# Kernel tuning notes

Hardware: AMD Instinct MI355X
Metric: run time of the kernel (lower is better)

The kernel has to match this reference:

```python
import jax, jax.numpy as jnp
import numpy as np

BM = 192          # query-group block size (kernel assert: mbm == 192)
TOPK = 896        # round(0.3 * n / 64) * 64 selected keys per query group
RAND_ONE_IN = 100


def setup_inputs() -> dict:
    key = jax.random.key(0)
    kq, kk, kv = jax.random.split(key, 3)
    b, h, n, d = 1, 24, 3072, 128
    q = jax.random.normal(kq, (b, h, n, d), dtype=jnp.float32)
    k = jax.random.normal(kk, (b, h, n, d), dtype=jnp.float32)
    v = jax.random.normal(kv, (b, h, n, d), dtype=jnp.float32)
    return {"q": q, "k": k, "v": v}


def reference(q, k, v):
    b, h, n, d = q.shape
    qg = n // BM
    scale = 1.0 / np.sqrt(d).astype(np.float32)
    # dense attention (dense_colsum_attn): output + per-query-group column sums
    s = jnp.einsum('bhqd,bhkd->bhqk', q, k) * scale          # [b,h,n,n]
    p = jax.nn.softmax(s, axis=-1)
    o = jnp.einsum('bhqk,bhkd->bhqd', p, v)                  # dense output
    cs = p.reshape(b, h, qg, BM, n).sum(axis=3)              # block colsums [b,h,qg,n]
    rmask = jax.random.randint(jax.random.key(1), cs.shape, 0, RAND_ONE_IN) == 0
    idx = jax.lax.top_k(cs, TOPK)[1]                         # [b,h,qg,TOPK]
    flat = rmask.reshape(-1, n)
    rows = jnp.arange(flat.shape[0])[:, None]
    mask = flat.at[rows, idx.reshape(-1, TOPK)].set(True).reshape(b, h, qg, n)
    # csp_attn: block-sparse attention, each BM-query group attends only to masked keys
    sg = s.reshape(b, h, qg, BM, n)
    neg = jnp.finfo(s.dtype).min
    sp_p = jax.nn.softmax(jnp.where(mask[:, :, :, None, :], sg, neg), axis=-1)
    sp = jnp.einsum('bhgmk,bhkd->bhgmd', sp_p, v).reshape(b, h, n, d)
    # full step returns o; out_cache (stored for sparse steps) is o - sp
    return jnp.stack([o, o - sp])  # [2,b,h,n,d]
```

## Files before the change

### kernel.cpp

```cpp
#include <hip/hip_runtime.h>
#include <math.h>

#define H  24
#define NN 3072
#define D  128
#define G  16
#define BM 192
#define TOPK_K 896
#define PST 34
#define OUT2_OFF ((size_t)H * NN * D)
#define KV_HALF_BYTES ((size_t)H * NN * D * 2)
#define CSD_BYTES ((size_t)H * G * NN * 8)

#define LOG2E_SCALE 0.12751743822f

typedef _Float16 half8 __attribute__((ext_vector_type(8)));
typedef _Float16 half4v __attribute__((ext_vector_type(4)));
typedef __fp16 fp16x2 __attribute__((ext_vector_type(2)));
typedef float floatx4 __attribute__((ext_vector_type(4)));

#define GLOAD_LDS(g, l) __builtin_amdgcn_global_load_lds( \
    (const __attribute__((address_space(1))) void*)(g),   \
    (__attribute__((address_space(3))) void*)(l), 16, 0, 0)
#define WAITVM(N) asm volatile("s_waitcnt vmcnt(" #N ")" ::: "memory")

__device__ __forceinline__ floatx4 fzero4() {
  floatx4 z = {0.f, 0.f, 0.f, 0.f};
  return z;
}
__device__ __forceinline__ half8 pack_h8_rte(float4 a, float4 b) {
  half8 r;
  r[0] = (_Float16)a.x; r[1] = (_Float16)a.y; r[2] = (_Float16)a.z; r[3] = (_Float16)a.w;
  r[4] = (_Float16)b.x; r[5] = (_Float16)b.y; r[6] = (_Float16)b.z; r[7] = (_Float16)b.w;
  return r;
}
__device__ __forceinline__ half8 pack_h8_rtz(float4 a, float4 b) {
  fp16x2 h0 = __builtin_amdgcn_cvt_pkrtz(a.x, a.y);
  fp16x2 h1 = __builtin_amdgcn_cvt_pkrtz(a.z, a.w);
  fp16x2 h2 = __builtin_amdgcn_cvt_pkrtz(b.x, b.y);
  fp16x2 h3 = __builtin_amdgcn_cvt_pkrtz(b.z, b.w);
  half8 r;
  r[0] = (_Float16)h0[0]; r[1] = (_Float16)h0[1];
  r[2] = (_Float16)h1[0]; r[3] = (_Float16)h1[1];
  r[4] = (_Float16)h2[0]; r[5] = (_Float16)h2[1];
  r[6] = (_Float16)h3[0]; r[7] = (_Float16)h3[1];
  return r;
}
__device__ __forceinline__ half8 pack_h8_residual(float4 a, float4 b, half8 hi) {
  float4 ra = make_float4(a.x - (float)hi[0], a.y - (float)hi[1],
                          a.z - (float)hi[2], a.w - (float)hi[3]);
  float4 rb = make_float4(b.x - (float)hi[4], b.y - (float)hi[5],
                          b.z - (float)hi[6], b.w - (float)hi[7]);
  return pack_h8_rte(ra, rb);
}

__device__ __forceinline__ void tf2x32(unsigned k0, unsigned k1, unsigned x0, unsigned x1,
                                       unsigned* o0, unsigned* o1) {
  unsigned ks2 = k0 ^ k1 ^ 0x1BD11BDAu;
  unsigned v0 = x0 + k0, v1 = x1 + k1;
#define TF_RND(r) { v0 += v1; v1 = (v1 << (r)) | (v1 >> (32 - (r))); v1 ^= v0; }
  TF_RND(13) TF_RND(15) TF_RND(26) TF_RND(6)   v0 += k1;  v1 += ks2 + 1u;
  TF_RND(17) TF_RND(29) TF_RND(16) TF_RND(24)  v0 += ks2; v1 += k0 + 2u;
  TF_RND(13) TF_RND(15) TF_RND(26) TF_RND(6)   v0 += k0;  v1 += k1 + 3u;
  TF_RND(17) TF_RND(29) TF_RND(16) TF_RND(24)  v0 += k1;  v1 += ks2 + 4u;
  TF_RND(13) TF_RND(15) TF_RND(26) TF_RND(6)   v0 += ks2; v1 += k0 + 5u;
#undef TF_RND
  *o0 = v0; *o1 = v1;
}

__global__ __launch_bounds__(256)
void rmask_kernel(float* __restrict__ mask) {
  const unsigned S = H * G * NN;
  unsigned i = blockIdx.x * 256u + threadIdx.x;
  if (i >= S) return;
  unsigned hb, lb, a, b;
  unsigned k1a, k1b, k2a, k2b;
  tf2x32(0u, 1u, 0u, 0u, &k1a, &k1b);
  tf2x32(0u, 1u, 0u, 1u, &k2a, &k2b);
  tf2x32(k1a, k1b, 0u, i, &a, &b); hb = a ^ b;
  tf2x32(k2a, k2b, 0u, i, &a, &b); lb = a ^ b;
  unsigned r = ((hb % 100u) * 96u + (lb % 100u)) % 100u;
  mask[i] = (r == 0u) ? 1.0f : 0.0f;
}

__global__ __launch_bounds__(256)
void cvt_k_kernel(const float* __restrict__ k, _Float16* __restrict__ khi,
                  _Float16* __restrict__ klo) {
  size_t i = (size_t)blockIdx.x * 256 + threadIdx.x;
  const float4* src = (const float4*)k + i * 2;
  float4 a = src[0], b = src[1];
  half8 hi = pack_h8_rte(a, b);
  *(half8*)(khi + i * 8) = hi;
  *(half8*)(klo + i * 8) = pack_h8_residual(a, b, hi);
}

__global__ __launch_bounds__(256)
void cvt_vT_kernel(const float* __restrict__ v, _Float16* __restrict__ vT) {
  __shared__ _Float16 t[64][68];
  const int h = blockIdx.z, k0 = blockIdx.x * 64, d0 = blockIdx.y * 64;
  const int tid = threadIdx.x;
  const int c4 = tid & 15, r = tid >> 4;
#pragma unroll
  for (int i = 0; i < 4; ++i) {
    int row = r + i * 16;
    float4 x = *(const float4*)(v + ((size_t)(h * NN + k0 + row)) * D + d0 + c4 * 4);
    t[c4 * 4 + 0][row] = (_Float16)x.x;
    t[c4 * 4 + 1][row] = (_Float16)x.y;
    t[c4 * 4 + 2][row] = (_Float16)x.z;
    t[c4 * 4 + 3][row] = (_Float16)x.w;
  }
  __syncthreads();
#pragma unroll
  for (int i = 0; i < 4; ++i) {
    int drow = r + i * 16;
    half4v val = *(const half4v*)&t[drow][c4 * 4];
    *(half4v*)(vT + (size_t)(h * D + d0 + drow) * NN + k0 + c4 * 4) = val;
  }
}

__global__ __launch_bounds__(256, 2)
void dense_kernel(const float* __restrict__ q, const _Float16* __restrict__ khi_g,
                  const _Float16* __restrict__ klo_g, const _Float16* __restrict__ vT,
                  float* __restrict__ out, double* __restrict__ csb) {
  __shared__ __align__(16) _Float16 skK[2][8192];
  __shared__ __align__(16) float p_sh[4][2][16 * PST];
  const int tid = threadIdx.x;
  const int wave = tid >> 6, lane = tid & 63;
  const int l15 = lane & 15, l4 = lane >> 4;
  const int wq = ((blockIdx.x & 7) * 72) + (blockIdx.x >> 3);
  const int h = wq / 24;
  const int m0 = (wq % 24) * 128;
  const int rowbase = m0 + wave * 32;
  const _Float16* khi = khi_g + (size_t)h * NN * D;
  const _Float16* klo = klo_g + (size_t)h * NN * D;
  const _Float16* vh = vT + (size_t)h * D * NN;

  const _Float16* ksrc = (wave < 2) ? khi : klo;
#define STAGE_K(kc_, buf_) {                                                    \
  _Pragma("unroll") for (int i_ = 0; i_ < 4; ++i_) {                            \
    int c_ = wave * 4 + i_;                                                     \
    int row_ = (c_ & 7) * 4 + l4;                                               \
    int gc_ = l15 ^ ((c_ & 1) * 4 + l4);                                        \
    GLOAD_LDS(ksrc + (size_t)((kc_) + row_) * D + gc_ * 8, &skK[buf_][c_ * 512]); \
  } }

  int kcol[4];
#pragma unroll
  for (int ds = 0; ds < 4; ++ds) kcol[ds] = ((ds * 4 + l4) ^ (l15 & 7)) * 8;

  half8 qh[2][4], ql[2][4];
#pragma unroll
  for (int mt = 0; mt < 2; ++mt)
#pragma unroll
    for (int ds = 0; ds < 4; ++ds) {
      const float* qp = q + ((size_t)(h * NN + rowbase + mt * 16 + l15)) * D + ds * 32 + l4 * 8;
      float4 a = *(const float4*)qp, b = *(const float4*)(qp + 4);
      qh[mt][ds] = pack_h8_rte(a, b);
      ql[mt][ds] = pack_h8_residual(a, b, qh[mt][ds]);
    }

  float Lacc[2][4] = {{0.f, 0.f, 0.f, 0.f}, {0.f, 0.f, 0.f, 0.f}};
  STAGE_K(0, 0)
#pragma unroll 1
  for (int t = 0; t < 96; ++t) {
    const int tn = ((t + 1) % 96) * 32;
    STAGE_K(tn, (t + 1) & 1)
    WAITVM(4);
    __builtin_amdgcn_s_barrier();
    const _Float16* bk = &skK[t & 1][0];
    floatx4 S[2][2];
#pragma unroll
    for (int mt = 0; mt < 2; ++mt)
#pragma unroll
      for (int nt = 0; nt < 2; ++nt) S[mt][nt] = fzero4();
#pragma unroll
    for (int nt = 0; nt < 2; ++nt) {
      const int rb = (nt * 16 + l15) * 128;
#pragma unroll
      for (int ds = 0; ds < 4; ++ds) {
        half8 kbh = *(const half8*)&bk[rb + kcol[ds]];
        half8 kbl = *(const half8*)&bk[4096 + rb + kcol[ds]];
        S[0][nt] = __builtin_amdgcn_mfma_f32_16x16x32_f16(qh[0][ds], kbh, S[0][nt], 0, 0, 0);
        S[1][nt] = __builtin_amdgcn_mfma_f32_16x16x32_f16(qh[1][ds], kbh, S[1][nt], 0, 0, 0);
        S[0][nt] = __builtin_amdgcn_mfma_f32_16x16x32_f16(qh[0][ds], kbl, S[0][nt], 0, 0, 0);
        S[1][nt] = __builtin_amdgcn_mfma_f32_16x16x32_f16(qh[1][ds], kbl, S[1][nt], 0, 0, 0);
        S[0][nt] = __builtin_amdgcn_mfma_f32_16x16x32_f16(ql[0][ds], kbh, S[0][nt], 0, 0, 0);
        S[1][nt] = __builtin_amdgcn_mfma_f32_16x16x32_f16(ql[1][ds], kbh, S[1][nt], 0, 0, 0);
      }
    }
#pragma unroll
    for (int mt = 0; mt < 2; ++mt)
#pragma unroll
      for (int nt = 0; nt < 2; ++nt)
#pragma unroll
        for (int r = 0; r < 4; ++r)
          Lacc[mt][r] += __builtin_amdgcn_exp2f(S[mt][nt][r] * LOG2E_SCALE);
    __builtin_amdgcn_s_barrier();
  }
  float invL[2][4];
  double dinvL[2][4];
#pragma unroll
  for (int mt = 0; mt < 2; ++mt)
#pragma unroll
    for (int r = 0; r < 4; ++r) {
      float x = Lacc[mt][r];
      x += __shfl_xor(x, 1); x += __shfl_xor(x, 2);
      x += __shfl_xor(x, 4); x += __shfl_xor(x, 8);
      invL[mt][r] = 1.0f / x;
      dinvL[mt][r] = (double)invL[mt][r];
    }

  double* csrow[2];
#pragma unroll
  for (int mt = 0; mt < 2; ++mt)
    csrow[mt] = csb + ((size_t)h * G + (rowbase + mt * 16) / BM) * NN;
  floatx4 O[2][8];
#pragma unroll
  for (int mt = 0; mt < 2; ++mt)
#pragma unroll
    for (int dt = 0; dt < 8; ++dt) O[mt][dt] = fzero4();

#pragma unroll 1
  for (int t = 0; t < 96; ++t) {
    const int kc = t * 32;
    const int tn = ((t + 1) % 96) * 32;
    STAGE_K(tn, (t + 1) & 1)
    WAITVM(4);
    __builtin_amdgcn_s_barrier();
    const _Float16* bk = &skK[t & 1][0];
    floatx4 S[2][2];
#pragma unroll
    for (int mt = 0; mt < 2; ++mt)
#pragma unroll
      for (int nt = 0; nt < 2; ++nt) S[mt][nt] = fzero4();
#pragma unroll
    for (int nt = 0; nt < 2; ++nt) {
      const int rb = (nt * 16 + l15) * 128;
#pragma unroll
      for (int ds = 0; ds < 4; ++ds) {
        half8 kbh = *(const half8*)&bk[rb + kcol[ds]];
        half8 kbl = *(const half8*)&bk[4096 + rb + kcol[ds]];
        S[0][nt] = __builtin_amdgcn_mfma_f32_16x16x32_f16(qh[0][ds], kbh, S[0][nt], 0, 0, 0);
        S[1][nt] = __builtin_amdgcn_mfma_f32_16x16x32_f16(qh[1][ds], kbh, S[1][nt], 0, 0, 0);
        S[0][nt] = __builtin_amdgcn_mfma_f32_16x16x32_f16(qh[0][ds], kbl, S[0][nt], 0, 0, 0);
        S[1][nt] = __builtin_amdgcn_mfma_f32_16x16x32_f16(qh[1][ds], kbl, S[1][nt], 0, 0, 0);
        S[0][nt] = __builtin_amdgcn_mfma_f32_16x16x32_f16(ql[0][ds], kbh, S[0][nt], 0, 0, 0);
        S[1][nt] = __builtin_amdgcn_mfma_f32_16x16x32_f16(ql[1][ds], kbh, S[1][nt], 0, 0, 0);
      }
    }
    half8 vb[8];
#pragma unroll
    for (int dt = 0; dt < 8; ++dt)
      vb[dt] = *(const half8*)(vh + (size_t)(dt * 16 + l15) * NN + kc + l4 * 8);
#pragma unroll
    for (int mt = 0; mt < 2; ++mt) {
      float* p_wave = &p_sh[wave][mt][0];
#pragma unroll
      for (int nt = 0; nt < 2; ++nt) {
        float e0 = __builtin_amdgcn_exp2f(S[mt][nt][0] * LOG2E_SCALE);
        float e1 = __builtin_amdgcn_exp2f(S[mt][nt][1] * LOG2E_SCALE);
        float e2 = __builtin_amdgcn_exp2f(S[mt][nt][2] * LOG2E_SCALE);
        float e3 = __builtin_amdgcn_exp2f(S[mt][nt][3] * LOG2E_SCALE);
        const int base = (l4 * 4) * PST + nt * 16 + l15;
        p_wave[base] = e0; p_wave[base + PST] = e1;
        p_wave[base + 2 * PST] = e2; p_wave[base + 3 * PST] = e3;
        double csp = (double)e0 * dinvL[mt][0] + (double)e1 * dinvL[mt][1]
                   + (double)e2 * dinvL[mt][2] + (double)e3 * dinvL[mt][3];
        csp += __shfl_xor(csp, 16);
        csp += __shfl_xor(csp, 32);
        if (lane < 16) atomicAdd(&csrow[mt][kc + nt * 16 + l15], csp);
      }
    }
    {
      half8 pa[2];
#pragma unroll
      for (int mt = 0; mt < 2; ++mt) {
        const float* pp = &p_sh[wave][mt][0] + l15 * PST + l4 * 8;
        pa[mt] = pack_h8_rtz(*(const float4*)pp, *(const float4*)(pp + 4));
      }
#pragma unroll
      for (int dt = 0; dt < 8; ++dt) {
        O[0][dt] = __builtin_amdgcn_mfma_f32_16x16x32_f16(pa[0], vb[dt], O[0][dt], 0, 0, 0);
        O[1][dt] = __builtin_amdgcn_mfma_f32_16x16x32_f16(pa[1], vb[dt], O[1][dt], 0, 0, 0);
      }
    }
    __builtin_amdgcn_s_barrier();
  }
#undef STAGE_K
  WAITVM(0);
#pragma unroll
  for (int mt = 0; mt < 2; ++mt)
#pragma unroll
    for (int dt = 0; dt < 8; ++dt)
#pragma unroll
      for (int r = 0; r < 4; ++r) {
        size_t idx = ((size_t)(h * NN + rowbase + mt * 16 + l4 * 4 + r)) * D + dt * 16 + l15;
        out[idx] = O[mt][dt][r] * invL[mt][r];
      }
}

__global__ __launch_bounds__(256)
void topk_kernel(const double* __restrict__ csb, float* __restrict__ maskb) {
  const int hg = blockIdx.x;
  const double* cs = csb + (size_t)hg * NN;
  float* mask = maskb + (size_t)hg * NN;
  __shared__ unsigned long long vals[NN];
  __shared__ int wsum[4];
  const int tid = threadIdx.x;
  for (int i = tid; i < NN; i += 256)
    vals[i] = (unsigned long long)__double_as_longlong(cs[i]);
  __syncthreads();
  unsigned long long T = 0ull;
  for (int b = 62; b >= 0; --b) {
    unsigned long long cand = T | (1ull << b);
    int c = 0;
    for (int i = tid; i < NN; i += 256) c += (vals[i] >= cand) ? 1 : 0;
#pragma unroll
    for (int off = 32; off; off >>= 1) c += __shfl_xor(c, off);
    if ((tid & 63) == 0) wsum[tid >> 6] = c;
    __syncthreads();
    int total = wsum[0] + wsum[1] + wsum[2] + wsum[3];
    if (total >= TOPK_K) T = cand;
    __syncthreads();
  }
  int c = 0;
  for (int i = tid; i < NN; i += 256) c += (vals[i] > T) ? 1 : 0;
#pragma unroll
  for (int off = 32; off; off >>= 1) c += __shfl_xor(c, off);
  if ((tid & 63) == 0) wsum[tid >> 6] = c;
  __syncthreads();
  int cgt = wsum[0] + wsum[1] + wsum[2] + wsum[3];
  int need = TOPK_K - cgt;
  for (int i = tid; i < NN; i += 256)
    if (vals[i] > T) mask[i] = 1.0f;
  __syncthreads();
  if (tid == 0) {
    int c2 = 0;
    for (int i = 0; i < NN && c2 < need; ++i)
      if (vals[i] == T) { mask[i] = 1.0f; ++c2; }
  }
}

__global__ __launch_bounds__(256, 3)
void sparse_kernel(const float* __restrict__ q, const _Float16* __restrict__ kf,
                   const _Float16* __restrict__ vT, const float* __restrict__ maskb,
                   float* __restrict__ out) {
  __shared__ __align__(16) _Float16 skK[2][4096];
  __shared__ __align__(16) float p_sh[4][2][16 * PST];
  const int tid = threadIdx.x;
  const int wave = tid >> 6, lane = tid & 63;
  const int l15 = lane & 15, l4 = lane >> 4;
  const int wq = ((blockIdx.x & 7) * 72) + (blockIdx.x >> 3);
  const int h = wq / 24;
  const int m0 = (wq % 24) * 128;
  const int rowbase = m0 + wave * 32;
  const _Float16* kh = kf + (size_t)h * NN * D;
  const _Float16* vh = vT + (size_t)h * D * NN;

#define SSTAGE(kc_, buf_) {                                                     \
  _Pragma("unroll") for (int i_ = 0; i_ < 2; ++i_) {                            \
    int c_ = wave * 2 + i_;                                                     \
    int row_ = c_ * 4 + l4;                                                     \
    int gc_ = l15 ^ ((c_ & 1) * 4 + l4);                                        \
    GLOAD_LDS(kh + (size_t)((kc_) + row_) * D + gc_ * 8, &skK[buf_][c_ * 512]); \
  } }

  int kcol[4];
#pragma unroll
  for (int ds = 0; ds < 4; ++ds) kcol[ds] = ((ds * 4 + l4) ^ (l15 & 7)) * 8;

  half8 qa[2][4];
#pragma unroll
  for (int mt = 0; mt < 2; ++mt)
#pragma unroll
    for (int ds = 0; ds < 4; ++ds) {
      const float* qp = q + ((size_t)(h * NN + rowbase + mt * 16 + l15)) * D + ds * 32 + l4 * 8;
      qa[mt][ds] = pack_h8_rte(*(const float4*)qp, *(const float4*)(qp + 4));
    }

  const float* mrow[2];
#pragma unroll
  for (int mt = 0; mt < 2; ++mt)
    mrow[mt] = maskb + ((size_t)h * G + (rowbase + mt * 16) / BM) * NN;

  float lacc[2][4] = {{0.f, 0.f, 0.f, 0.f}, {0.f, 0.f, 0.f, 0.f}};
  floatx4 O[2][8];
#pragma unroll
  for (int mt = 0; mt < 2; ++mt)
#pragma unroll
    for (int dt = 0; dt < 8; ++dt) O[mt][dt] = fzero4();

  SSTAGE(0, 0)
#pragma unroll 1
  for (int t = 0; t < 96; ++t) {
    const int kc = t * 32;
    const int tn = ((t + 1) % 96) * 32;
    SSTAGE(tn, (t + 1) & 1)
    WAITVM(2);
    __builtin_amdgcn_s_barrier();
    const _Float16* bk = &skK[t & 1][0];
    float mv[2][2];
#pragma unroll
    for (int mt = 0; mt < 2; ++mt)
#pragma unroll
      for (int nt = 0; nt < 2; ++nt) mv[mt][nt] = mrow[mt][kc + nt * 16 + l15];
    floatx4 S[2][2];
#pragma unroll
    for (int mt = 0; mt < 2; ++mt)
#pragma unroll
      for (int nt = 0; nt < 2; ++nt) S[mt][nt] = fzero4();
#pragma unroll
    for (int nt = 0; nt < 2; ++nt) {
      const int rb = (nt * 16 + l15) * 128;
#pragma unroll
      for (int ds = 0; ds < 4; ++ds) {
        half8 kb = *(const half8*)&bk[rb + kcol[ds]];
        S[0][nt] = __builtin_amdgcn_mfma_f32_16x16x32_f16(qa[0][ds], kb, S[0][nt], 0, 0, 0);
        S[1][nt] = __builtin_amdgcn_mfma_f32_16x16x32_f16(qa[1][ds], kb, S[1][nt], 0, 0, 0);
      }
    }
    half8 vb[8];
#pragma unroll
    for (int dt = 0; dt < 8; ++dt)
      vb[dt] = *(const half8*)(vh + (size_t)(dt * 16 + l15) * NN + kc + l4 * 8);
#pragma unroll
    for (int mt = 0; mt < 2; ++mt) {
      float* p_wave = &p_sh[wave][mt][0];
#pragma unroll
      for (int nt = 0; nt < 2; ++nt) {
        float e0 = __builtin_amdgcn_exp2f(S[mt][nt][0] * LOG2E_SCALE) * mv[mt][nt];
        float e1 = __builtin_amdgcn_exp2f(S[mt][nt][1] * LOG2E_SCALE) * mv[mt][nt];
        float e2 = __builtin_amdgcn_exp2f(S[mt][nt][2] * LOG2E_SCALE) * mv[mt][nt];
        float e3 = __builtin_amdgcn_exp2f(S[mt][nt][3] * LOG2E_SCALE) * mv[mt][nt];
        lacc[mt][0] += e0; lacc[mt][1] += e1; lacc[mt][2] += e2; lacc[mt][3] += e3;
        const int base = (l4 * 4) * PST + nt * 16 + l15;
        p_wave[base] = e0; p_wave[base + PST] = e1;
        p_wave[base + 2 * PST] = e2; p_wave[base + 3 * PST] = e3;
      }
    }
    {
      half8 pa[2];
#pragma unroll
      for (int mt = 0; mt < 2; ++mt) {
        const float* pp = &p_sh[wave][mt][0] + l15 * PST + l4 * 8;
        pa[mt] = pack_h8_rtz(*(const float4*)pp, *(const float4*)(pp + 4));
      }
#pragma unroll
      for (int dt = 0; dt < 8; ++dt) {
        O[0][dt] = __builtin_amdgcn_mfma_f32_16x16x32_f16(pa[0], vb[dt], O[0][dt], 0, 0, 0);
        O[1][dt] = __builtin_amdgcn_mfma_f32_16x16x32_f16(pa[1], vb[dt], O[1][dt], 0, 0, 0);
      }
    }
    __builtin_amdgcn_s_barrier();
  }
#undef SSTAGE
  WAITVM(0);
  float invl[2][4];
#pragma unroll
  for (int mt = 0; mt < 2; ++mt)
#pragma unroll
    for (int r = 0; r < 4; ++r) {
      float x = lacc[mt][r];
      x += __shfl_xor(x, 1); x += __shfl_xor(x, 2);
      x += __shfl_xor(x, 4); x += __shfl_xor(x, 8);
      invl[mt][r] = 1.0f / x;
    }
#pragma unroll
  for (int mt = 0; mt < 2; ++mt)
#pragma unroll
    for (int dt = 0; dt < 8; ++dt)
#pragma unroll
      for (int r = 0; r < 4; ++r) {
        size_t idx = ((size_t)(h * NN + rowbase + mt * 16 + l4 * 4 + r)) * D + dt * 16 + l15;
        out[OUT2_OFF + idx] = out[idx] - O[mt][dt][r] * invl[mt][r];
      }
}

extern "C" void kernel_launch(void* const* d_in, const int* in_sizes, int n_in,
                              void* d_out, int out_size, void* d_ws, size_t ws_size,
                              hipStream_t stream) {
  const float* q = (const float*)d_in[0];
  const float* k = (const float*)d_in[1];
  const float* v = (const float*)d_in[2];
  float* out = (float*)d_out;
  char* wsb = (char*)d_ws;

  _Float16* khi = (_Float16*)wsb;
  _Float16* klo = (_Float16*)(wsb + KV_HALF_BYTES);
  _Float16* vT  = (_Float16*)(wsb + 2 * KV_HALF_BYTES);
  double* csb   = (double*)(wsb + 3 * KV_HALF_BYTES);
  float* maskb  = (float*)(wsb + 3 * KV_HALF_BYTES + CSD_BYTES);

  (void)hipMemsetAsync(csb, 0, CSD_BYTES, stream);
  cvt_k_kernel<<<dim3((H * NN * D) / (8 * 256)), dim3(256), 0, stream>>>(k, khi, klo);
  cvt_vT_kernel<<<dim3(NN / 64, D / 64, H), dim3(256), 0, stream>>>(v, vT);
  rmask_kernel<<<dim3(H * G * NN / 256), dim3(256), 0, stream>>>(maskb);
  dense_kernel<<<dim3((NN / 128) * H), dim3(256), 0, stream>>>(q, khi, klo, vT, out, csb);
  topk_kernel<<<dim3(H * G), dim3(256), 0, stream>>>(csb, maskb);
  sparse_kernel<<<dim3((NN / 128) * H), dim3(256), 0, stream>>>(q, khi, vT, maskb, out);
}
```

Before: 1.360 ms.

## Reorder loads and split softmax/PV per row tile to overlap memory with compute

```diff
diff --git a/kernel.cpp b/kernel.cpp
--- a/kernel.cpp
+++ b/kernel.cpp
@@ -224,8 +224,11 @@
   for (int t = 0; t < 96; ++t) {
     const int kc = t * 32;
     const int tn = ((t + 1) % 96) * 32;
-    STAGE_K(tn, (t + 1) & 1)
-    WAITVM(4);
+    half8 vb[8];
+#pragma unroll
+    for (int dt = 0; dt < 8; ++dt)
+      vb[dt] = *(const half8*)(vh + (size_t)(dt * 16 + l15) * NN + kc + l4 * 8);
+    WAITVM(8);
     __builtin_amdgcn_s_barrier();
     const _Float16* bk = &skK[t & 1][0];
     floatx4 S[2][2];
@@ -248,41 +251,57 @@
         S[1][nt] = __builtin_amdgcn_mfma_f32_16x16x32_f16(ql[1][ds], kbh, S[1][nt], 0, 0, 0);
       }
     }
-    half8 vb[8];
-#pragma unroll
-    for (int dt = 0; dt < 8; ++dt)
-      vb[dt] = *(const half8*)(vh + (size_t)(dt * 16 + l15) * NN + kc + l4 * 8);
-#pragma unroll
-    for (int mt = 0; mt < 2; ++mt) {
-      float* p_wave = &p_sh[wave][mt][0];
+    STAGE_K(tn, (t + 1) & 1)
+    {
+      float* p_wave = &p_sh[wave][0][0];
 #pragma unroll
       for (int nt = 0; nt < 2; ++nt) {
-        float e0 = __builtin_amdgcn_exp2f(S[mt][nt][0] * LOG2E_SCALE);
-        float e1 = __builtin_amdgcn_exp2f(S[mt][nt][1] * LOG2E_SCALE);
-        float e2 = __builtin_amdgcn_exp2f(S[mt][nt][2] * LOG2E_SCALE);
-        float e3 = __builtin_amdgcn_exp2f(S[mt][nt][3] * LOG2E_SCALE);
+        float e0 = __builtin_amdgcn_exp2f(S[0][nt][0] * LOG2E_SCALE);
+        float e1 = __builtin_amdgcn_exp2f(S[0][nt][1] * LOG2E_SCALE);
+        float e2 = __builtin_amdgcn_exp2f(S[0][nt][2] * LOG2E_SCALE);
+        float e3 = __builtin_amdgcn_exp2f(S[0][nt][3] * LOG2E_SCALE);
         const int base = (l4 * 4) * PST + nt * 16 + l15;
         p_wave[base] = e0; p_wave[base + PST] = e1;
         p_wave[base + 2 * PST] = e2; p_wave[base + 3 * PST] = e3;
-        double csp = (double)e0 * dinvL[mt][0] + (double)e1 * dinvL[mt][1]
-                   + (double)e2 * dinvL[mt][2] + (double)e3 * dinvL[mt][3];
+        double csp = (double)e0 * dinvL[0][0] + (double)e1 * dinvL[0][1]
+                   + (double)e2 * dinvL[0][2] + (double)e3 * dinvL[0][3];
         csp += __shfl_xor(csp, 16);
         csp += __shfl_xor(csp, 32);
-        if (lane < 16) atomicAdd(&csrow[mt][kc + nt * 16 + l15], csp);
-      }
-    }
-    {
-      half8 pa[2];
-#pragma unroll
-      for (int mt = 0; mt < 2; ++mt) {
-        const float* pp = &p_sh[wave][mt][0] + l15 * PST + l4 * 8;
-        pa[mt] = pack_h8_rtz(*(const float4*)pp, *(const float4*)(pp + 4));
-      }
-#pragma unroll
-      for (int dt = 0; dt < 8; ++dt) {
-        O[0][dt] = __builtin_amdgcn_mfma_f32_16x16x32_f16(pa[0], vb[dt], O[0][dt], 0, 0, 0);
-        O[1][dt] = __builtin_amdgcn_mfma_f32_16x16x32_f16(pa[1], vb[dt], O[1][dt], 0, 0, 0);
-      }
+        if (lane < 16) atomicAdd(&csrow[0][kc + nt * 16 + l15], csp);
+      }
+    }
+    WAITVM(6);
+    {
+      const float* pp = &p_sh[wave][0][0] + l15 * PST + l4 * 8;
+      half8 pa = pack_h8_rtz(*(const float4*)pp, *(const float4*)(pp + 4));
+#pragma unroll
+      for (int dt = 0; dt < 8; ++dt)
+        O[0][dt] = __builtin_amdgcn_mfma_f32_16x16x32_f16(pa, vb[dt], O[0][dt], 0, 0, 0);
+    }
+    {
+      float* p_wave = &p_sh[wave][1][0];
+#pragma unroll
+      for (int nt = 0; nt < 2; ++nt) {
+        float e0 = __builtin_amdgcn_exp2f(S[1][nt][0] * LOG2E_SCALE);
+        float e1 = __builtin_amdgcn_exp2f(S[1][nt][1] * LOG2E_SCALE);
+        float e2 = __builtin_amdgcn_exp2f(S[1][nt][2] * LOG2E_SCALE);
+        float e3 = __builtin_amdgcn_exp2f(S[1][nt][3] * LOG2E_SCALE);
+        const int base = (l4 * 4) * PST + nt * 16 + l15;
+        p_wave[base] = e0; p_wave[base + PST] = e1;
+        p_wave[base + 2 * PST] = e2; p_wave[base + 3 * PST] = e3;
+        double csp = (double)e0 * dinvL[1][0] + (double)e1 * dinvL[1][1]
+                   + (double)e2 * dinvL[1][2] + (double)e3 * dinvL[1][3];
+        csp += __shfl_xor(csp, 16);
+        csp += __shfl_xor(csp, 32);
+        if (lane < 16) atomicAdd(&csrow[1][kc + nt * 16 + l15], csp);
+      }
+    }
+    {
+      const float* pp = &p_sh[wave][1][0] + l15 * PST + l4 * 8;
+      half8 pa = pack_h8_rtz(*(const float4*)pp, *(const float4*)(pp + 4));
+#pragma unroll
+      for (int dt = 0; dt < 8; ++dt)
+        O[1][dt] = __builtin_amdgcn_mfma_f32_16x16x32_f16(pa, vb[dt], O[1][dt], 0, 0, 0);
     }
     __builtin_amdgcn_s_barrier();
   }
@@ -395,15 +414,18 @@
   for (int t = 0; t < 96; ++t) {
     const int kc = t * 32;
     const int tn = ((t + 1) % 96) * 32;
-    SSTAGE(tn, (t + 1) & 1)
-    WAITVM(2);
+    float mv[2][2];
+#pragma unroll
+    for (int mt = 0; mt < 2; ++mt)
+#pragma unroll
+      for (int nt = 0; nt < 2; ++nt) mv[mt][nt] = mrow[mt][kc + nt * 16 + l15];
+    half8 vb[8];
+#pragma unroll
+    for (int dt = 0; dt < 8; ++dt)
+      vb[dt] = *(const half8*)(vh + (size_t)(dt * 16 + l15) * NN + kc + l4 * 8);
+    WAITVM(12);
     __builtin_amdgcn_s_barrier();
     const _Float16* bk = &skK[t & 1][0];
-    float mv[2][2];
-#pragma unroll
-    for (int mt = 0; mt < 2; ++mt)
-#pragma unroll
-      for (int nt = 0; nt < 2; ++nt) mv[mt][nt] = mrow[mt][kc + nt * 16 + l15];
     floatx4 S[2][2];
 #pragma unroll
     for (int mt = 0; mt < 2; ++mt)
@@ -419,37 +441,50 @@
         S[1][nt] = __builtin_amdgcn_mfma_f32_16x16x32_f16(qa[1][ds], kb, S[1][nt], 0, 0, 0);
       }
     }
-    half8 vb[8];
-#pragma unroll
-    for (int dt = 0; dt < 8; ++dt)
-      vb[dt] = *(const half8*)(vh + (size_t)(dt * 16 + l15) * NN + kc + l4 * 8);
-#pragma unroll
-    for (int mt = 0; mt < 2; ++mt) {
-      float* p_wave = &p_sh[wave][mt][0];
+    SSTAGE(tn, (t + 1) & 1)
+    WAITVM(10);
+    {
+      float* p_wave = &p_sh[wave][0][0];
 #pragma unroll
       for (int nt = 0; nt < 2; ++nt) {
-        float e0 = __builtin_amdgcn_exp2f(S[mt][nt][0] * LOG2E_SCALE) * mv[mt][nt];
-        float e1 = __builtin_amdgcn_exp2f(S[mt][nt][1] * LOG2E_SCALE) * mv[mt][nt];
-        float e2 = __builtin_amdgcn_exp2f(S[mt][nt][2] * LOG2E_SCALE) * mv[mt][nt];
-        float e3 = __builtin_amdgcn_exp2f(S[mt][nt][3] * LOG2E_SCALE) * mv[mt][nt];
-        lacc[mt][0] += e0; lacc[mt][1] += e1; lacc[mt][2] += e2; lacc[mt][3] += e3;
+        float e0 = __builtin_amdgcn_exp2f(S[0][nt][0] * LOG2E_SCALE) * mv[0][nt];
+        float e1 = __builtin_amdgcn_exp2f(S[0][nt][1] * LOG2E_SCALE) * mv[0][nt];
+        float e2 = __builtin_amdgcn_exp2f(S[0][nt][2] * LOG2E_SCALE) * mv[0][nt];
+        float e3 = __builtin_amdgcn_exp2f(S[0][nt][3] * LOG2E_SCALE) * mv[0][nt];
+        lacc[0][0] += e0; lacc[0][1] += e1; lacc[0][2] += e2; lacc[0][3] += e3;
         const int base = (l4 * 4) * PST + nt * 16 + l15;
         p_wave[base] = e0; p_wave[base + PST] = e1;
         p_wave[base + 2 * PST] = e2; p_wave[base + 3 * PST] = e3;
       }
     }
-    {
-      half8 pa[2];
-#pragma unroll
-      for (int mt = 0; mt < 2; ++mt) {
-        const float* pp = &p_sh[wave][mt][0] + l15 * PST + l4 * 8;
-        pa[mt] = pack_h8_rtz(*(const float4*)pp, *(const float4*)(pp + 4));
-      }
-#pragma unroll
-      for (int dt = 0; dt < 8; ++dt) {
-        O[0][dt] = __builtin_amdgcn_mfma_f32_16x16x32_f16(pa[0], vb[dt], O[0][dt], 0, 0, 0);
-        O[1][dt] = __builtin_amdgcn_mfma_f32_16x16x32_f16(pa[1], vb[dt], O[1][dt], 0, 0, 0);
-      }
+    WAITVM(2);
+    {
+      const float* pp = &p_sh[wave][0][0] + l15 * PST + l4 * 8;
+      half8 pa = pack_h8_rtz(*(const float4*)pp, *(const float4*)(pp + 4));
+#pragma unroll
+      for (int dt = 0; dt < 8; ++dt)
+        O[0][dt] = __builtin_amdgcn_mfma_f32_16x16x32_f16(pa, vb[dt], O[0][dt], 0, 0, 0);
+    }
+    {
+      float* p_wave = &p_sh[wave][1][0];
+#pragma unroll
+      for (int nt = 0; nt < 2; ++nt) {
+        float e0 = __builtin_amdgcn_exp2f(S[1][nt][0] * LOG2E_SCALE) * mv[1][nt];
+        float e1 = __builtin_amdgcn_exp2f(S[1][nt][1] * LOG2E_SCALE) * mv[1][nt];
+        float e2 = __builtin_amdgcn_exp2f(S[1][nt][2] * LOG2E_SCALE) * mv[1][nt];
+        float e3 = __builtin_amdgcn_exp2f(S[1][nt][3] * LOG2E_SCALE) * mv[1][nt];
+        lacc[1][0] += e0; lacc[1][1] += e1; lacc[1][2] += e2; lacc[1][3] += e3;
+        const int base = (l4 * 4) * PST + nt * 16 + l15;
+        p_wave[base] = e0; p_wave[base + PST] = e1;
+        p_wave[base + 2 * PST] = e2; p_wave[base + 3 * PST] = e3;
+      }
+    }
+    {
+      const float* pp = &p_sh[wave][1][0] + l15 * PST + l4 * 8;
+      half8 pa = pack_h8_rtz(*(const float4*)pp, *(const float4*)(pp + 4));
+#pragma unroll
+      for (int dt = 0; dt < 8; ++dt)
+        O[1][dt] = __builtin_amdgcn_mfma_f32_16x16x32_f16(pa, vb[dt], O[1][dt], 0, 0, 0);
     }
     __builtin_amdgcn_s_barrier();
   }
```

New measurement: 1.534 ms. 12.8% more time.
